# Kernel tuning notes

Measured on AMD Instinct MI355X. Metric: run time of the kernel, lower is better.

Reference implementation:

```python
import jax, jax.numpy as jnp
import numpy as np

H = 16  # num_heads

def _rotate_half(x):
    x1, x2 = jnp.split(x, 2, axis=-1)
    return jnp.concatenate((-x2, x1), axis=-1)

def setup_inputs() -> dict:
    key = jax.random.key(0)
    ks = jax.random.split(key, 8)
    B, N, C = 4, 2048, 1024
    d = C // H
    x = jax.random.normal(ks[0], (B, N, C), dtype=jnp.float32)
    cos = jax.random.uniform(ks[1], (1, 1, N, d), dtype=jnp.float32)
    sin = jax.random.uniform(ks[2], (1, 1, N, d), dtype=jnp.float32)
    s = 0.02
    Wq = jax.random.normal(ks[3], (C, C), dtype=jnp.float32) * s
    Wkv = jax.random.normal(ks[4], (C, 2 * C), dtype=jnp.float32) * s
    Wout = jax.random.normal(ks[5], (C, C), dtype=jnp.float32) * s
    bout = jnp.zeros((C,), dtype=jnp.float32)
    return {"x": x, "cos": cos, "sin": sin, "Wq": Wq, "Wkv": Wkv, "Wout": Wout, "bout": bout}

def reference(x, cos, sin, Wq, Wkv, Wout, bout):
    B, N, C = x.shape
    d = C // H
    scale = d ** (-0.5)
    # projections (qkv_bias=False)
    q = (x @ Wq).reshape(B, N, H, d).transpose(0, 2, 1, 3)        # (B,H,N,d)
    kv = x @ Wkv                                                   # (B,N,2C)
    k, v = jnp.split(kv, 2, axis=-1)
    k = k.reshape(B, N, H, d).transpose(0, 2, 1, 3)
    v = v.reshape(B, N, H, d).transpose(0, 2, 1, 3)
    # inline RoPE
    q = q * cos + _rotate_half(q) * sin
    k = k * cos + _rotate_half(k) * sin
    # naive full attention
    sim = jnp.einsum('bhid,bhjd->bhij', q, k) * scale              # (B,H,N,N)
    attn = jax.nn.softmax(sim, axis=-1)
    out = jnp.einsum('bhij,bhjd->bhid', attn, v)                   # (B,H,N,d)
    out = out.transpose(0, 2, 1, 3).reshape(B, N, C)
    return out @ Wout + bout
```

## Files before the change

### kernel.cpp

```cpp
#include <hip/hip_runtime.h>


typedef unsigned short u16;
typedef unsigned int u32;
typedef __attribute__((ext_vector_type(4))) short s16x4;
typedef __attribute__((ext_vector_type(8))) short short8;
typedef __attribute__((ext_vector_type(8))) unsigned short ushort8;
typedef __attribute__((ext_vector_type(4))) float f32x4;

#define MFMA16x16x32 __builtin_amdgcn_mfma_f32_16x16x32_bf16
#define QSCALE 0.180336880434135f

#if __has_builtin(__builtin_amdgcn_exp2f)
#define EXP2F __builtin_amdgcn_exp2f
#else
#define EXP2F exp2f
#endif

__device__ __forceinline__ float b2f(u16 u) {
  union { u32 i; float f; } x; x.i = ((u32)u) << 16; return x.f;
}
__device__ __forceinline__ u16 f2b(float f) {
  union { float f; u32 i; } x; x.f = f;
  u32 r = (x.i + 0x7FFFu + ((x.i >> 16) & 1u)) >> 16;
  return (u16)r;
}
__device__ __forceinline__ u32 f2b_trunc32(float f) {
  union { float f; u32 i; } x; x.f = f;
  return x.i >> 16;
}
__device__ __forceinline__ bool detect_f32(const u32* __restrict__ cw) {
  u32 acc = 0;
#pragma unroll
  for (int i = 0; i < 64; ++i) acc |= cw[i];
  return (acc & 0x8000u) != 0;
}
__device__ __forceinline__ float ldval(const void* p, long i, bool f32) {
  return f32 ? ((const float*)p)[i] : b2f(((const u16*)p)[i]);
}
__device__ __forceinline__ ushort8 ld8f(const float* p) {
  float4 u0 = *(const float4*)p;
  float4 u1 = *(const float4*)(p + 4);
  ushort8 r;
  r[0] = f2b(u0.x); r[1] = f2b(u0.y); r[2] = f2b(u0.z); r[3] = f2b(u0.w);
  r[4] = f2b(u1.x); r[5] = f2b(u1.y); r[6] = f2b(u1.z); r[7] = f2b(u1.w);
  return r;
}
__device__ __forceinline__ void async16(const void* g, void* l) {
  __builtin_amdgcn_global_load_lds((const __attribute__((address_space(1))) void*)g,
                                   (__attribute__((address_space(3))) void*)l, 16, 0, 0);
}

__global__ __launch_bounds__(256)
void convert_x(const void* __restrict__ src, u16* __restrict__ dst,
               const u32* __restrict__ cosw) {
  const bool f32 = detect_f32(cosw);
  const long i = ((long)blockIdx.x * 256 + threadIdx.x) * 8;
  ushort8 v;
  if (f32) v = ld8f((const float*)src + i);
  else     v = *(const ushort8*)((const u16*)src + i);
  *(ushort8*)(dst + i) = v;
}

__global__ __launch_bounds__(256)
void transpose_any(const void* __restrict__ src, u16* __restrict__ dst,
                   int R, int C, const u32* __restrict__ cosw) {
  const bool f32 = detect_f32(cosw);
  const int tr = blockIdx.y * 64, tc = blockIdx.x * 64;
  __shared__ __align__(16) u16 tile[64][65];
  const int t = threadIdx.x;
#pragma unroll
  for (int i = 0; i < 2; ++i) {
    const int ch = i * 256 + t;
    const int r = ch >> 3, cc = ch & 7;
    ushort8 v;
    if (f32) v = ld8f((const float*)src + (long)(tr + r) * C + tc + cc * 8);
    else     v = *(const ushort8*)((const u16*)src + (long)(tr + r) * C + tc + cc * 8);
#pragma unroll
    for (int j = 0; j < 8; ++j) tile[r][cc * 8 + j] = v[j];
  }
  __syncthreads();
#pragma unroll
  for (int i = 0; i < 2; ++i) {
    const int ch = i * 256 + t;
    const int c = ch >> 3, rc = ch & 7;
    ushort8 v;
#pragma unroll
    for (int j = 0; j < 8; ++j) v[j] = tile[rc * 8 + j][c];
    *(ushort8*)(dst + (long)(tc + c) * R + tr + rc * 8) = v;
  }
}

__global__ __launch_bounds__(256)
void transpose_b16(const u16* __restrict__ src, u16* __restrict__ dst,
                   int R, int C, long sb, long db) {
  src += (long)blockIdx.z * sb;
  dst += (long)blockIdx.z * db;
  const int tr = blockIdx.y * 64, tc = blockIdx.x * 64;
  __shared__ __align__(16) u16 tile[64][65];
  const int t = threadIdx.x;
#pragma unroll
  for (int i = 0; i < 2; ++i) {
    const int ch = i * 256 + t;
    const int r = ch >> 3, cc = ch & 7;
    ushort8 v = *(const ushort8*)(src + (long)(tr + r) * C + tc + cc * 8);
#pragma unroll
    for (int j = 0; j < 8; ++j) tile[r][cc * 8 + j] = v[j];
  }
  __syncthreads();
#pragma unroll
  for (int i = 0; i < 2; ++i) {
    const int ch = i * 256 + t;
    const int c = ch >> 3, rc = ch & 7;
    ushort8 v;
#pragma unroll
    for (int j = 0; j < 8; ++j) v[j] = tile[rc * 8 + j][c];
    *(ushort8*)(dst + (long)(tc + c) * R + tr + rc * 8) = v;
  }
}

template <int MODE>
__global__ __launch_bounds__(256)
void gemm_fast(const u16* __restrict__ A, const u16* __restrict__ BT,
               const void* cosp, const void* sinp,
               u16* q_ws, u16* k_ws, u16* v_ws,
               const void* bias, void* outp, const u32* __restrict__ cosw) {
  constexpr int K = 1024, ITERS = K / 32;
  constexpr int NBX = (MODE == 0) ? 24 : 8;
  __shared__ __align__(16) u16 As[2][128 * 32];
  __shared__ __align__(16) u16 Bs[2][128 * 32];
  const int tid = threadIdx.x;
  const int wave = tid >> 6, lane = tid & 63;
  const int quad = lane >> 4, l15 = lane & 15;
  const int mh = (wave >> 1) * 64, nh = (wave & 1) * 64;
  const f32x4 zero4 = {0.f, 0.f, 0.f, 0.f};

  const int w = blockIdx.y * NBX + blockIdx.x;
  const int xcd = w & 7, idx = w >> 3;
  int bx, by;
  if (MODE == 0) {
    const int xc = idx / 48, r = idx % 48;
    by = xcd * 8 + r / 6;
    bx = xc * 6 + r % 6;
  } else {
    by = xcd * 8 + idx / 8;
    bx = idx % 8;
  }
  const int m0 = by * 128, n0 = bx * 128;

  f32x4 acc[4][4];
#pragma unroll
  for (int i = 0; i < 4; ++i)
#pragma unroll
    for (int j = 0; j < 4; ++j) acc[i][j] = zero4;

  const int c0 = tid, c1 = 256 + tid;
  const u16* a0p = A  + (long)(m0 + (c0 >> 2)) * K + (((c0 & 3) ^ ((c0 >> 3) & 3)) * 8);
  const u16* a1p = A  + (long)(m0 + (c1 >> 2)) * K + (((c1 & 3) ^ ((c1 >> 3) & 3)) * 8);
  const u16* b0p = BT + (long)(n0 + (c0 >> 2)) * K + (((c0 & 3) ^ ((c0 >> 3) & 3)) * 8);
  const u16* b1p = BT + (long)(n0 + (c1 >> 2)) * K + (((c1 & 3) ^ ((c1 >> 3) & 3)) * 8);

#define STAGE(buf, kt)                                \
  do {                                                \
    async16(a0p + (kt), As[buf] + c0 * 8);            \
    async16(a1p + (kt), As[buf] + c1 * 8);            \
    async16(b0p + (kt), Bs[buf] + c0 * 8);            \
    async16(b1p + (kt), Bs[buf] + c1 * 8);            \
  } while (0)

  const int rk = (quad ^ ((l15 >> 1) & 3)) * 8;

  STAGE(0, 0);
  for (int it = 0; it < ITERS; ++it) {
    const int cur = it & 1;
    __syncthreads();
    if (it + 1 < ITERS) STAGE(cur ^ 1, (it + 1) * 32);
    short8 af[4], bf[4];
#pragma unroll
    for (int s = 0; s < 4; ++s) {
      af[s] = *(const short8*)(As[cur] + (mh + s * 16 + l15) * 32 + rk);
      bf[s] = *(const short8*)(Bs[cur] + (nh + s * 16 + l15) * 32 + rk);
    }
#pragma unroll
    for (int i = 0; i < 4; ++i)
#pragma unroll
      for (int j = 0; j < 4; ++j)
        acc[i][j] = MFMA16x16x32(af[i], bf[j], acc[i][j], 0, 0, 0);
  }
#undef STAGE

  const bool f32 = detect_f32(cosw);

  if (MODE == 0) {
    const int seg = n0 >> 10;
    const int csbase = (n0 & 1023) + nh;
    u16* segp = (seg == 0) ? q_ws : (seg == 1) ? k_ws : v_ws;
#pragma unroll
    for (int i = 0; i < 4; ++i) {
#pragma unroll
      for (int r = 0; r < 4; ++r) {
        const int mm = m0 + mh + i * 16 + quad * 4 + r;
        const int b = mm >> 11, n = mm & 2047;
#pragma unroll
        for (int j = 0; j < 4; ++j) {
          const int cs = csbase + j * 16 + l15;
          const int h = cs >> 6, dv = cs & 63;
          float val = acc[i][j][r];
          if (seg < 2) {
            const float cv = ldval(cosp, (long)n * 64 + dv, f32);
            const float sv = ldval(sinp, (long)n * 64 + dv, f32);
            const float part = acc[i][j ^ 2][r];
            val = val * cv + ((dv < 32) ? -part : part) * sv;
            if (seg == 0) val *= QSCALE;
          }
          segp[(((long)(b * 16 + h) * 2048 + n) << 6) + dv] = f2b(val);
        }
      }
    }
  } else {
#pragma unroll
    for (int i = 0; i < 4; ++i) {
#pragma unroll
      for (int r = 0; r < 4; ++r) {
        const int mm = m0 + mh + i * 16 + quad * 4 + r;
#pragma unroll
        for (int j = 0; j < 4; ++j) {
          const int cc = n0 + nh + j * 16 + l15;
          const float val = acc[i][j][r] + ldval(bias, cc, f32);
          if (f32) ((float*)outp)[(long)mm * 1024 + cc] = val;
          else     ((u16*)outp)[(long)mm * 1024 + cc] = f2b(val);
        }
      }
    }
  }
}

__global__ __launch_bounds__(512, 4)
void flash_k(const u16* __restrict__ q_ws, const u16* __restrict__ k_ws,
             const u16* __restrict__ vT_ws, u16* __restrict__ attn) {
  __shared__ __align__(16) u16 Ks[2][64 * 64];
  __shared__ __align__(16) u16 Vts[2][64 * 64];
  const int tid = threadIdx.x, wave = tid >> 6, lane = tid & 63;
  const int quad = lane >> 4, l15 = lane & 15;
  const int s7 = l15 & 7;
  const int bid = blockIdx.x + (blockIdx.y << 3);
  const int qx = bid >> 6;
  const int bh = ((bid & 7) << 3) | ((bid >> 3) & 7);
  const int qr0 = qx * 256 + wave * 32;
  const u16* Q  = q_ws  + (long)bh * 2048 * 64;
  const u16* Kp = k_ws  + (long)bh * 2048 * 64;
  const u16* Vt = vT_ws + (long)bh * 64 * 2048;
  const f32x4 zero4 = {0.f, 0.f, 0.f, 0.f};
  short8 ones;
#pragma unroll
  for (int i = 0; i < 8; ++i) ones[i] = (short)0x3F80;

  short8 aq[2][2];
#pragma unroll
  for (int ms = 0; ms < 2; ++ms)
#pragma unroll
    for (int ks = 0; ks < 2; ++ks)
      aq[ms][ks] = *(const short8*)(Q + (long)(qr0 + ms * 16 + l15) * 64 + ks * 32 + quad * 8);

  f32x4 accO[2][4], accL[2];
#pragma unroll
  for (int ms = 0; ms < 2; ++ms) {
#pragma unroll
    for (int jd = 0; jd < 4; ++jd) accO[ms][jd] = zero4;
    accL[ms] = zero4;
  }

  const int rr = tid >> 3, gg = ((tid & 7) ^ (rr & 7)) * 8;

#define STAGEKV(buf, kt)                                          \
  do {                                                            \
    async16(Kp + (long)((kt) + rr) * 64 + gg, Ks[buf] + tid * 8); \
    async16(Vt + (long)rr * 2048 + (kt) + gg, Vts[buf] + tid * 8);\
  } while (0)

  const int vh = (quad & 1) * 4;
  const int vc0a = ((0 + (quad >> 1)) ^ s7) * 8 + vh;
  const int vc0b = ((2 + (quad >> 1)) ^ s7) * 8 + vh;
  const int vc1a = ((4 + (quad >> 1)) ^ s7) * 8 + vh;
  const int vc1b = ((6 + (quad >> 1)) ^ s7) * 8 + vh;

  STAGEKV(0, 0);
  for (int it = 0; it < 32; ++it) {
    const int cur = it & 1;
    __syncthreads();
    if (it + 1 < 32) STAGEKV(cur ^ 1, (it + 1) * 64);

#pragma unroll
    for (int k2 = 0; k2 < 2; ++k2) {
      u32 pk[2][4];
#pragma unroll
      for (int nsl = 0; nsl < 2; ++nsl) {
        const int ns = k2 * 2 + nsl;
        const u16* rowK = Ks[cur] + (ns * 16 + l15) * 64;
        short8 b0 = *(const short8*)(rowK + ((quad ^ s7) * 8));
        short8 b1 = *(const short8*)(rowK + (((quad + 4) ^ s7) * 8));
#pragma unroll
        for (int ms = 0; ms < 2; ++ms) {
          f32x4 t = MFMA16x16x32(b0, aq[ms][0], zero4, 0, 0, 0);
          f32x4 sa = MFMA16x16x32(b1, aq[ms][1], t, 0, 0, 0);
          const u32 p0 = f2b_trunc32(EXP2F(sa[0]));
          const u32 p1 = f2b_trunc32(EXP2F(sa[1]));
          const u32 p2 = f2b_trunc32(EXP2F(sa[2]));
          const u32 p3 = f2b_trunc32(EXP2F(sa[3]));
          pk[ms][nsl * 2 + 0] = p0 | (p1 << 16);
          pk[ms][nsl * 2 + 1] = p2 | (p3 << 16);
        }
      }
      short8 ap[2];
#pragma unroll
      for (int ms = 0; ms < 2; ++ms) {
        union { u32 w[4]; short8 s; } u;
        u.w[0] = pk[ms][0]; u.w[1] = pk[ms][1];
        u.w[2] = pk[ms][2]; u.w[3] = pk[ms][3];
        ap[ms] = u.s;
        accL[ms] = MFMA16x16x32(ap[ms], ones, accL[ms], 0, 0, 0);
      }
      const int ca = k2 ? vc1a : vc0a;
      const int cb = k2 ? vc1b : vc0b;
#pragma unroll
      for (int jd = 0; jd < 4; ++jd) {
        const u16* rowV = Vts[cur] + (jd * 16 + l15) * 64;
        union { s16x4 h[2]; short8 s; } bv;
        bv.h[0] = *(const s16x4*)(rowV + ca);
        bv.h[1] = *(const s16x4*)(rowV + cb);
#pragma unroll
        for (int ms = 0; ms < 2; ++ms)
          accO[ms][jd] = MFMA16x16x32(ap[ms], bv.s, accO[ms][jd], 0, 0, 0);
      }
    }
  }
#undef STAGEKV

  const int b = bh >> 4, h = bh & 15;
#pragma unroll
  for (int ms = 0; ms < 2; ++ms) {
#pragma unroll
    for (int r = 0; r < 4; ++r) {
      const float inv = 1.f / accL[ms][r];
      const int row = qr0 + ms * 16 + quad * 4 + r;
#pragma unroll
      for (int jd = 0; jd < 4; ++jd) {
        const int cc = h * 64 + jd * 16 + l15;
        attn[((long)(b * 2048 + row)) * 1024 + cc] = f2b(accO[ms][jd][r] * inv);
      }
    }
  }
}

extern "C" void kernel_launch(void* const* d_in, const int* in_sizes, int n_in,
                              void* d_out, int out_size, void* d_ws, size_t ws_size,
                              hipStream_t stream) {
  const void* x    = d_in[0];
  const void* cosp = d_in[1];
  const void* sinp = d_in[2];
  const void* Wq   = d_in[3];
  const void* Wkv  = d_in[4];
  const void* Wout = d_in[5];
  const void* bout = d_in[6];
  const u32* cosw  = (const u32*)d_in[1];

  char* ws = (char*)d_ws;
  const size_t MB = 1u << 20;
  u16* q_ws  = (u16*)(ws);
  u16* k_ws  = (u16*)(ws + 16 * MB);
  u16* vT_ws = (u16*)(ws + 32 * MB);
  u16* v_ws  = (u16*)(ws + 48 * MB);
  u16* attn  = (u16*)(ws + 48 * MB);
  u16* WoutT = (u16*)(ws + 32 * MB);

  u16* WT1;
  if (ws_size >= 88 * MB) WT1 = (u16*)(ws + 64 * MB);
  else                    WT1 = (u16*)d_out;
  u16* x_bf16 = WT1 + 3072 * 1024;

  convert_x<<<dim3(4096), 256, 0, stream>>>(x, x_bf16, cosw);
  transpose_any<<<dim3(16, 16), 256, 0, stream>>>(Wq, WT1, 1024, 1024, cosw);
  transpose_any<<<dim3(32, 16), 256, 0, stream>>>(Wkv, WT1 + 1024 * 1024, 1024, 2048, cosw);
  gemm_fast<0><<<dim3(24, 64), 256, 0, stream>>>(x_bf16, WT1, cosp, sinp,
                                                 q_ws, k_ws, v_ws,
                                                 nullptr, nullptr, cosw);
  transpose_b16<<<dim3(1, 32, 64), 256, 0, stream>>>(v_ws, vT_ws, 2048, 64,
                                                     (long)2048 * 64, (long)64 * 2048);
  flash_k<<<dim3(8, 64), 512, 0, stream>>>(q_ws, k_ws, vT_ws, attn);
  transpose_any<<<dim3(16, 16), 256, 0, stream>>>(Wout, WoutT, 1024, 1024, cosw);
  gemm_fast<1><<<dim3(8, 64), 256, 0, stream>>>(attn, WoutT, cosp, sinp,
                                                nullptr, nullptr, nullptr,
                                                bout, d_out, cosw);
}
```

Measured before the change: 312.5 us.

## Triple-buffer K/V staging in flash kernel and merge prep kernels into one launch

The flash attention kernel moves from double to triple buffered K/V LDS staging, prefetching two tiles ahead. It uses explicit vmcnt waits with a raw barrier in place of __syncthreads, so global loads overlap more with the MFMA work. Separately, the x conversion and the two weight transposes are fused into a single prep launch to cut launch overhead. The extra LDS (48KB per block) may lower occupancy, and correctness depends on the vmcnt counts matching the number of outstanding async loads.

```diff
diff --git a/kernel.cpp b/kernel.cpp
--- a/kernel.cpp
+++ b/kernel.cpp
@@ -16,6 +16,10 @@
 #else
 #define EXP2F exp2f
 #endif
+
+#define GBAR() __builtin_amdgcn_s_barrier()
+#define CFENCE() asm volatile("" ::: "memory")
+#define WAITVM(n) asm volatile("s_waitcnt vmcnt(" #n ")" ::: "memory")
 
 __device__ __forceinline__ float b2f(u16 u) {
   union { u32 i; float f; } x; x.i = ((u32)u) << 16; return x.f;
@@ -52,14 +56,52 @@
 }
 
 __global__ __launch_bounds__(256)
-void convert_x(const void* __restrict__ src, u16* __restrict__ dst,
-               const u32* __restrict__ cosw) {
+void prep(const void* __restrict__ x, u16* __restrict__ x_bf16,
+          const void* __restrict__ Wq, const void* __restrict__ Wkv,
+          u16* __restrict__ WT1, const u32* __restrict__ cosw) {
   const bool f32 = detect_f32(cosw);
-  const long i = ((long)blockIdx.x * 256 + threadIdx.x) * 8;
-  ushort8 v;
-  if (f32) v = ld8f((const float*)src + i);
-  else     v = *(const ushort8*)((const u16*)src + i);
-  *(ushort8*)(dst + i) = v;
+  const int b = blockIdx.x;
+  const int t = threadIdx.x;
+  if (b < 4096) {
+    const long i = ((long)b * 256 + t) * 8;
+    ushort8 v;
+    if (f32) v = ld8f((const float*)x + i);
+    else     v = *(const ushort8*)((const u16*)x + i);
+    *(ushort8*)(x_bf16 + i) = v;
+    return;
+  }
+  __shared__ __align__(16) u16 tile[64][65];
+  const void* src; u16* dst; int R, C, bx, by;
+  if (b < 4352) {
+    const int idx = b - 4096;
+    src = Wq;  dst = WT1;               R = 1024; C = 1024;
+    bx = idx & 15; by = idx >> 4;
+  } else {
+    const int idx = b - 4352;
+    src = Wkv; dst = WT1 + 1024 * 1024; R = 1024; C = 2048;
+    bx = idx & 31; by = idx >> 5;
+  }
+  const int tr = by * 64, tc = bx * 64;
+#pragma unroll
+  for (int i = 0; i < 2; ++i) {
+    const int ch = i * 256 + t;
+    const int r = ch >> 3, cc = ch & 7;
+    ushort8 v;
+    if (f32) v = ld8f((const float*)src + (long)(tr + r) * C + tc + cc * 8);
+    else     v = *(const ushort8*)((const u16*)src + (long)(tr + r) * C + tc + cc * 8);
+#pragma unroll
+    for (int j = 0; j < 8; ++j) tile[r][cc * 8 + j] = v[j];
+  }
+  __syncthreads();
+#pragma unroll
+  for (int i = 0; i < 2; ++i) {
+    const int ch = i * 256 + t;
+    const int c = ch >> 3, rc = ch & 7;
+    ushort8 v;
+#pragma unroll
+    for (int j = 0; j < 8; ++j) v[j] = tile[rc * 8 + j][c];
+    *(ushort8*)(dst + (long)(tc + c) * R + tr + rc * 8) = v;
+  }
 }
 
 __global__ __launch_bounds__(256)
@@ -238,8 +280,8 @@
 __global__ __launch_bounds__(512, 4)
 void flash_k(const u16* __restrict__ q_ws, const u16* __restrict__ k_ws,
              const u16* __restrict__ vT_ws, u16* __restrict__ attn) {
-  __shared__ __align__(16) u16 Ks[2][64 * 64];
-  __shared__ __align__(16) u16 Vts[2][64 * 64];
+  __shared__ __align__(16) u16 Ks[3][64 * 64];
+  __shared__ __align__(16) u16 Vts[3][64 * 64];
   const int tid = threadIdx.x, wave = tid >> 6, lane = tid & 63;
   const int quad = lane >> 4, l15 = lane & 15;
   const int s7 = l15 & 7;
@@ -285,10 +327,12 @@
   const int vc1b = ((6 + (quad >> 1)) ^ s7) * 8 + vh;
 
   STAGEKV(0, 0);
+  STAGEKV(1, 64);
   for (int it = 0; it < 32; ++it) {
-    const int cur = it & 1;
-    __syncthreads();
-    if (it + 1 < 32) STAGEKV(cur ^ 1, (it + 1) * 64);
+    const int cur = it % 3;
+    if (it + 1 < 32) { WAITVM(2); } else { WAITVM(0); }
+    GBAR(); CFENCE();
+    if (it + 2 < 32) STAGEKV((it + 2) % 3, (it + 2) * 64);
 
 #pragma unroll
     for (int k2 = 0; k2 < 2; ++k2) {
@@ -378,9 +422,7 @@
   else                    WT1 = (u16*)d_out;
   u16* x_bf16 = WT1 + 3072 * 1024;
 
-  convert_x<<<dim3(4096), 256, 0, stream>>>(x, x_bf16, cosw);
-  transpose_any<<<dim3(16, 16), 256, 0, stream>>>(Wq, WT1, 1024, 1024, cosw);
-  transpose_any<<<dim3(32, 16), 256, 0, stream>>>(Wkv, WT1 + 1024 * 1024, 1024, 2048, cosw);
+  prep<<<dim3(4864), 256, 0, stream>>>(x, x_bf16, Wq, Wkv, WT1, cosw);
   gemm_fast<0><<<dim3(24, 64), 256, 0, stream>>>(x_bf16, WT1, cosp, sinp,
                                                  q_ws, k_ws, v_ws,
                                                  nullptr, nullptr, cosw);
```

Result: no change. 312.4 us (-0.0%).
